# Optimization experiments

Hardware: AMD Instinct MI355X
Metric: run time of the kernel (lower is better)

The kernel has to match this reference:

```python
import jax, jax.numpy as jnp
import numpy as np

V, E, H, O = 50000, 300, 1024, 5
B, T = 64, 512


def setup_inputs() -> dict:
    key = jax.random.key(0)
    ks = jax.random.split(key, 8)
    s_ih = 1.0 / np.sqrt(H)
    return {
        "x": jax.random.randint(ks[0], (B, T), 0, V, dtype=jnp.int32),
        "embeddings": jax.random.normal(ks[1], (V, E), dtype=jnp.float32),
        "W_ih": jax.random.uniform(ks[2], (3 * H, E), jnp.float32, -s_ih, s_ih),
        "W_hh": jax.random.uniform(ks[3], (3 * H, H), jnp.float32, -s_ih, s_ih),
        "b_ih": jax.random.uniform(ks[4], (3 * H,), jnp.float32, -s_ih, s_ih),
        "b_hh": jax.random.uniform(ks[5], (3 * H,), jnp.float32, -s_ih, s_ih),
        "W_fc": jax.random.uniform(ks[6], (O, H), jnp.float32, -s_ih, s_ih),
        "b_fc": jax.random.uniform(ks[7], (O,), jnp.float32, -s_ih, s_ih),
    }


def _gru_last_hidden(emb, W_ih, W_hh, b_ih, b_hh):
    # emb: [B, T, E] -> last hidden state [B, H]
    Hd = W_hh.shape[1]
    # Precompute input contributions for all timesteps: [B, T, 3H]
    gx_all = jnp.einsum("bte,ge->btg", emb, W_ih) + b_ih
    gx_all = jnp.swapaxes(gx_all, 0, 1)  # [T, B, 3H] for scan

    def step(h, gx):
        gh = h @ W_hh.T + b_hh  # [B, 3H]
        xr, xz, xn = jnp.split(gx, 3, axis=-1)
        hr, hz, hn = jnp.split(gh, 3, axis=-1)
        r = jax.nn.sigmoid(xr + hr)
        z = jax.nn.sigmoid(xz + hz)
        n = jnp.tanh(xn + r * hn)
        h_new = (1.0 - z) * n + z * h
        return h_new, None

    h0 = jnp.zeros((emb.shape[0], Hd), dtype=emb.dtype)
    h_last, _ = jax.lax.scan(step, h0, gx_all)
    return h_last


def reference(x, embeddings, W_ih, W_hh, b_ih, b_hh, W_fc, b_fc):
    emb = embeddings[x]  # [B, T, E] embedding lookup (frozen table)
    h_last = _gru_last_hidden(emb, W_ih, W_hh, b_ih, b_hh)  # [B, H]
    return h_last @ W_fc.T + b_fc  # [B, O]
```

## Files before the change

### kernel.cpp

```cpp
#include <hip/hip_runtime.h>
#include <hip/hip_bf16.h>

typedef unsigned short u16;
typedef unsigned long long u64;
typedef __attribute__((ext_vector_type(8))) short bf16x8;
typedef __attribute__((ext_vector_type(4))) float f32x4;

#define MFMA16(a, b, c) __builtin_amdgcn_mfma_f32_16x16x32_bf16((a), (b), (c), 0, 0, 0)

static constexpr int Ee = 300, EP = 320, Hh = 1024, G3 = 3072;
static constexpr int Bb = 64, Tt = 512;

static constexpr long OFF_GX   = 0L;
static constexpr long OFF_EMB  = 201326592L;
static constexpr long OFF_WIH  = 222298112L;
static constexpr long OFF_WHH  = 224264192L;
static constexpr long OFF_HBUF = 230555648L;
static constexpr long OFF_FLAG = 230817792L;

__device__ __forceinline__ u16 f2bf(float f) {
    union { float f; unsigned u; } v; v.f = f;
    unsigned u = v.u;
    return (u16)((u + 0x7fffu + ((u >> 16) & 1u)) >> 16);
}
__device__ __forceinline__ float bf2f(u16 u) {
    union { unsigned u; float f; } v; v.u = ((unsigned)u) << 16;
    return v.f;
}
__device__ __forceinline__ float fast_sigmoid(float x) {
    return 1.f / (1.f + __expf(-x));
}
__device__ __forceinline__ float fast_tanh(float x) {
    float ax = fabsf(x);
    float e = __expf(-2.f * ax);
    float t = (1.f - e) / (1.f + e);
    return copysignf(t, x);
}

static constexpr long R0 = (long)Bb * Tt * EP;
static constexpr long R1 = (long)G3 * EP;
static constexpr long R2 = (long)G3 * Hh;
static constexpr long R3 = 131072;
static constexpr long R4 = 1024;
static constexpr long R5 = 320;

__global__ void prep_kernel(const int* __restrict__ x, const float* __restrict__ emb,
                            const float* __restrict__ wih, const float* __restrict__ whh,
                            const float* __restrict__ bfc,
                            u16* __restrict__ emb_bf, u16* __restrict__ wih_bf,
                            u16* __restrict__ whh_bf, u16* __restrict__ h0,
                            int* __restrict__ cnt, float* __restrict__ out) {
    const long total = R0 + R1 + R2 + R3 + R4 + R5;
    for (long i = (long)blockIdx.x * blockDim.x + threadIdx.x; i < total;
         i += (long)gridDim.x * blockDim.x) {
        if (i < R0) {
            const int m = (int)(i / EP), k = (int)(i % EP);
            const int b = m & 63, t = m >> 6;
            u16 v = 0;
            if (k < Ee) {
                const int xi = x[b * Tt + t];
                v = f2bf(emb[(size_t)xi * Ee + k]);
            }
            emb_bf[i] = v;
        } else if (i < R0 + R1) {
            const long j = i - R0;
            const int k = (int)(j % EP);
            const int n = (int)(j / EP);
            wih_bf[j] = (k < Ee) ? f2bf(wih[(size_t)n * Ee + k]) : (u16)0;
        } else if (i < R0 + R1 + R2) {
            const long j = i - R0 - R1;
            whh_bf[j] = f2bf(whh[j]);
        } else if (i < R0 + R1 + R2 + R3) {
            h0[i - R0 - R1 - R2] = 0;
        } else if (i < R0 + R1 + R2 + R3 + R4) {
            cnt[i - R0 - R1 - R2 - R3] = 0;
        } else {
            const long j = i - R0 - R1 - R2 - R3 - R4;
            out[j] = bfc[j % 5];
        }
    }
}

__global__ __launch_bounds__(256, 2)
void gx_gemm(const u16* __restrict__ A, const u16* __restrict__ Bm,
             const float* __restrict__ bih, u16* __restrict__ gx) {
    __shared__ __align__(16) u16 lA[128 * 32];
    __shared__ __align__(16) u16 lB[128 * 32];
    const int tid = threadIdx.x;
    const int lane = tid & 63;
    const int wv = tid >> 6;
    const int quad = lane >> 4, l15 = lane & 15;
    const int m0 = blockIdx.x * 128;
    const int n0 = blockIdx.y * 128;
    const int mo = (wv & 1) * 64, no = (wv >> 1) * 64;
    const int srow = tid >> 2;
    const int sseg = tid & 3;

    f32x4 acc[4][4] = {};

    for (int s = 0; s < 10; ++s) {
        const int k0 = s * 32;
        __syncthreads();
#pragma unroll
        for (int p = 0; p < 2; ++p) {
            const u16* ga = A + (size_t)(m0 + p * 64 + srow) * EP + k0 + sseg * 8;
            u16* la = &lA[p * 2048 + wv * 512];
            __builtin_amdgcn_global_load_lds(
                (const __attribute__((address_space(1))) void*)ga,
                (__attribute__((address_space(3))) void*)la, 16, 0, 0);
            const u16* gb = Bm + (size_t)(n0 + p * 64 + srow) * EP + k0 + sseg * 8;
            u16* lb = &lB[p * 2048 + wv * 512];
            __builtin_amdgcn_global_load_lds(
                (const __attribute__((address_space(1))) void*)gb,
                (__attribute__((address_space(3))) void*)lb, 16, 0, 0);
        }
        __syncthreads();

        bf16x8 af[4], bfr[4];
#pragma unroll
        for (int mt = 0; mt < 4; ++mt)
            af[mt] = *(const bf16x8*)&lA[(mo + mt * 16 + l15) * 32 + quad * 8];
#pragma unroll
        for (int nt = 0; nt < 4; ++nt)
            bfr[nt] = *(const bf16x8*)&lB[(no + nt * 16 + l15) * 32 + quad * 8];
#pragma unroll
        for (int mt = 0; mt < 4; ++mt)
#pragma unroll
            for (int nt = 0; nt < 4; ++nt)
                acc[mt][nt] = MFMA16(af[mt], bfr[nt], acc[mt][nt]);
    }

#pragma unroll
    for (int mt = 0; mt < 4; ++mt) {
        const int mg = m0 + mo + mt * 16 + quad * 4;
        const int t = mg >> 6, b0 = mg & 63;
#pragma unroll
        for (int nt = 0; nt < 4; ++nt) {
            const int n = n0 + no + nt * 16 + l15;
            const float bi = bih[n];
            ushort4 vv;
            vv.x = f2bf(acc[mt][nt][0] + bi);
            vv.y = f2bf(acc[mt][nt][1] + bi);
            vv.z = f2bf(acc[mt][nt][2] + bi);
            vv.w = f2bf(acc[mt][nt][3] + bi);
            *(ushort4*)&gx[((size_t)t * G3 + n) * 64 + b0] = vv;
        }
    }
}

__global__ __launch_bounds__(512, 2)
void scan_kernel(const u16* __restrict__ whh, const float* __restrict__ bhh,
                 const u16* __restrict__ gx, u16* __restrict__ hbuf,
                 const float* __restrict__ wfc, float* __restrict__ out,
                 int* __restrict__ cnt) {
    __shared__ __align__(16) u16 lh[16 * 1032];
    __shared__ __align__(16) float red[2][3][4][256];

    const int bid = blockIdx.x;
    const int bg = bid >> 5;
    const int cg = bid & 31;
    const int w = threadIdx.x >> 6;
    const int lane = threadIdx.x & 63;
    const int kq = w & 3;
    const int nh = w >> 2;
    const int quad = lane >> 4, l15 = lane & 15;
    const int c0 = cg * 32;
    const bool isLoader = (nh == 0);
    const bool isGate = (w == 3) || (w == 4);
    const int gnh = (w == 3) ? 0 : 1;

    bf16x8 wf[3][8];
#pragma unroll
    for (int g = 0; g < 3; ++g) {
        const size_t rbase = (size_t)(g * 1024 + c0 + nh * 16 + l15) * 1024;
#pragma unroll
        for (int s = 0; s < 8; ++s)
            wf[g][s] = *(const bf16x8*)&whh[rbase + (kq * 8 + s) * 32 + quad * 8];
    }

    float bh[3][4];
    u16 gxv[3][4];
    float hO[4] = {0.f, 0.f, 0.f, 0.f};
    if (isGate) {
#pragma unroll
        for (int g = 0; g < 3; ++g)
#pragma unroll
            for (int jj = 0; jj < 4; ++jj) {
                const int jglob = c0 + gnh * 16 + quad * 4 + jj;
                bh[g][jj] = bhh[g * 1024 + jglob];
                gxv[g][jj] = gx[((size_t)0 * G3 + g * 1024 + jglob) * 64 + bg * 16 + l15];
            }
    }

    u16* hb = hbuf + bg * 32768;
    int* mycnt = &cnt[bg * 16];

    for (int t = 0; t < 512; ++t) {
        const u16* hc = hb + (t & 1) * 16384;
        u16* hn = hb + ((t + 1) & 1) * 16384;

        if (isLoader) {
            u64 stg[16];
            const u64* src = (const u64*)hc + kq * 1024 + lane;
#pragma unroll
            for (int r = 0; r < 16; ++r)
                stg[r] = __hip_atomic_load(src + r * 64, __ATOMIC_RELAXED,
                                           __HIP_MEMORY_SCOPE_AGENT);
#pragma unroll
            for (int r = 0; r < 16; ++r) {
                const int row = kq * 4 + (r >> 2);
                const int col = (r & 3) * 256 + lane * 4;
                *(u64*)&lh[row * 1032 + col] = stg[r];
            }
        }
        __syncthreads();

        bf16x8 af[8];
#pragma unroll
        for (int s = 0; s < 8; ++s)
            af[s] = *(const bf16x8*)&lh[l15 * 1032 + kq * 256 + s * 32 + quad * 8];
        f32x4 acc[3] = {};
#pragma unroll
        for (int s = 0; s < 8; ++s) {
            acc[0] = MFMA16(af[s], wf[0][s], acc[0]);
            acc[1] = MFMA16(af[s], wf[1][s], acc[1]);
            acc[2] = MFMA16(af[s], wf[2][s], acc[2]);
        }
#pragma unroll
        for (int g = 0; g < 3; ++g)
            *(f32x4*)&red[nh][g][kq][quad * 64 + l15 * 4] = acc[g];
        __syncthreads();

        if (isGate) {
            const int eb = (l15 >> 2) * 64 + quad * 16 + (l15 & 3);
            u64 pack = 0;
#pragma unroll
            for (int jj = 0; jj < 4; ++jj) {
                const int e = eb + jj * 4;
                const float s0 = red[gnh][0][0][e] + red[gnh][0][1][e] +
                                 red[gnh][0][2][e] + red[gnh][0][3][e];
                const float s1 = red[gnh][1][0][e] + red[gnh][1][1][e] +
                                 red[gnh][1][2][e] + red[gnh][1][3][e];
                const float s2 = red[gnh][2][0][e] + red[gnh][2][1][e] +
                                 red[gnh][2][2][e] + red[gnh][2][3][e];
                const float rg = fast_sigmoid(bf2f(gxv[0][jj]) + s0 + bh[0][jj]);
                const float zg = fast_sigmoid(bf2f(gxv[1][jj]) + s1 + bh[1][jj]);
                const float ng = fast_tanh(bf2f(gxv[2][jj]) + rg * (s2 + bh[2][jj]));
                const float hv = (1.f - zg) * ng + zg * hO[jj];
                hO[jj] = hv;
                pack |= (u64)f2bf(hv) << (jj * 16);
            }
            __hip_atomic_store((u64*)&hn[l15 * 1024 + c0 + gnh * 16 + quad * 4],
                               pack, __ATOMIC_RELAXED, __HIP_MEMORY_SCOPE_AGENT);
            if (t < 511) {
#pragma unroll
                for (int g = 0; g < 3; ++g)
#pragma unroll
                    for (int jj = 0; jj < 4; ++jj)
                        gxv[g][jj] = gx[((size_t)(t + 1) * G3 + g * 1024 + c0 +
                                         gnh * 16 + quad * 4 + jj) * 64 + bg * 16 + l15];
            }
        }
        __syncthreads();
        if (threadIdx.x == 0) atomicAdd(mycnt, 1);
        if (isLoader && t < 511) {
            if (lane == 0) {
                while (__hip_atomic_load(mycnt, __ATOMIC_RELAXED,
                                         __HIP_MEMORY_SCOPE_AGENT) < 32 * (t + 1)) {}
            }
        }
    }

    if (isGate) {
#pragma unroll
        for (int p = 0; p < 5; ++p) {
            float v = 0.f;
#pragma unroll
            for (int jj = 0; jj < 4; ++jj)
                v += hO[jj] * wfc[p * 1024 + c0 + gnh * 16 + quad * 4 + jj];
            v += __shfl_xor(v, 16);
            v += __shfl_xor(v, 32);
            if (quad == 0)
                atomicAdd(&out[(bg * 16 + l15) * 5 + p], v);
        }
    }
}

extern "C" void kernel_launch(void* const* d_in, const int* in_sizes, int n_in,
                              void* d_out, int out_size, void* d_ws, size_t ws_size,
                              hipStream_t stream) {
    const int*   x   = (const int*)d_in[0];
    const float* emb = (const float*)d_in[1];
    const float* wih = (const float*)d_in[2];
    const float* whh = (const float*)d_in[3];
    const float* bih = (const float*)d_in[4];
    const float* bhh = (const float*)d_in[5];
    const float* wfc = (const float*)d_in[6];
    const float* bfc = (const float*)d_in[7];
    float* out = (float*)d_out;

    char* ws = (char*)d_ws;
    u16*   gxw   = (u16*)(ws + OFF_GX);
    u16*   embbf = (u16*)(ws + OFF_EMB);
    u16*   wihbf = (u16*)(ws + OFF_WIH);
    u16*   whhbf = (u16*)(ws + OFF_WHH);
    u16*   hbuf  = (u16*)(ws + OFF_HBUF);
    int*   cnt   = (int*)(ws + OFF_FLAG);

    prep_kernel<<<8192, 256, 0, stream>>>(x, emb, wih, whh, bfc, embbf, wihbf,
                                          whhbf, hbuf, cnt, out);

    gx_gemm<<<dim3(256, 24), 256, 0, stream>>>(embbf, wihbf, bih, gxw);

    scan_kernel<<<128, 512, 0, stream>>>(whhbf, bhh, gxw, hbuf, wfc, out, cnt);
}
```

Baseline: 2.326 ms.

## Replace counter barrier with tag bits embedded in hidden-state words

Drops the global atomic counter and spin-wait between timesteps. Each packed 4-element hidden-state word now carries a parity tag in the LSB of its first bf16, and all threads poll their own words until the tag matches. This folds data and flag into one load. The reduction buffer is also padded and read as vectors, and all 512 threads share the loading. The cost is a perturbed LSB of one bf16 per group, which adds a little precision error, and more threads polling global memory.

New measurement: 2.645 ms. 1.14x slower.

```diff
diff --git a/kernel.cpp b/kernel.cpp
--- a/kernel.cpp
+++ b/kernel.cpp
@@ -16,7 +16,6 @@
 static constexpr long OFF_WIH  = 222298112L;
 static constexpr long OFF_WHH  = 224264192L;
 static constexpr long OFF_HBUF = 230555648L;
-static constexpr long OFF_FLAG = 230817792L;
 
 __device__ __forceinline__ u16 f2bf(float f) {
     union { float f; unsigned u; } v; v.f = f;
@@ -41,16 +40,15 @@
 static constexpr long R1 = (long)G3 * EP;
 static constexpr long R2 = (long)G3 * Hh;
 static constexpr long R3 = 131072;
-static constexpr long R4 = 1024;
-static constexpr long R5 = 320;
+static constexpr long R4 = 320;
 
 __global__ void prep_kernel(const int* __restrict__ x, const float* __restrict__ emb,
                             const float* __restrict__ wih, const float* __restrict__ whh,
                             const float* __restrict__ bfc,
                             u16* __restrict__ emb_bf, u16* __restrict__ wih_bf,
                             u16* __restrict__ whh_bf, u16* __restrict__ h0,
-                            int* __restrict__ cnt, float* __restrict__ out) {
-    const long total = R0 + R1 + R2 + R3 + R4 + R5;
+                            float* __restrict__ out) {
+    const long total = R0 + R1 + R2 + R3 + R4;
     for (long i = (long)blockIdx.x * blockDim.x + threadIdx.x; i < total;
          i += (long)gridDim.x * blockDim.x) {
         if (i < R0) {
@@ -71,11 +69,11 @@
             const long j = i - R0 - R1;
             whh_bf[j] = f2bf(whh[j]);
         } else if (i < R0 + R1 + R2 + R3) {
-            h0[i - R0 - R1 - R2] = 0;
-        } else if (i < R0 + R1 + R2 + R3 + R4) {
-            cnt[i - R0 - R1 - R2 - R3] = 0;
+            const long idx = i - R0 - R1 - R2;
+            const int slot = (int)((idx >> 14) & 1);
+            h0[idx] = (slot == 1 && (idx & 3) == 0) ? (u16)1 : (u16)0;
         } else {
-            const long j = i - R0 - R1 - R2 - R3 - R4;
+            const long j = i - R0 - R1 - R2 - R3;
             out[j] = bfc[j % 5];
         }
     }
@@ -151,10 +149,9 @@
 __global__ __launch_bounds__(512, 2)
 void scan_kernel(const u16* __restrict__ whh, const float* __restrict__ bhh,
                  const u16* __restrict__ gx, u16* __restrict__ hbuf,
-                 const float* __restrict__ wfc, float* __restrict__ out,
-                 int* __restrict__ cnt) {
+                 const float* __restrict__ wfc, float* __restrict__ out) {
     __shared__ __align__(16) u16 lh[16 * 1032];
-    __shared__ __align__(16) float red[2][3][4][256];
+    __shared__ __align__(16) float red[2][3][4][16 * 20];
 
     const int bid = blockIdx.x;
     const int bg = bid >> 5;
@@ -165,7 +162,6 @@
     const int nh = w >> 2;
     const int quad = lane >> 4, l15 = lane & 15;
     const int c0 = cg * 32;
-    const bool isLoader = (nh == 0);
     const bool isGate = (w == 3) || (w == 4);
     const int gnh = (w == 3) ? 0 : 1;
 
@@ -188,31 +184,38 @@
             for (int jj = 0; jj < 4; ++jj) {
                 const int jglob = c0 + gnh * 16 + quad * 4 + jj;
                 bh[g][jj] = bhh[g * 1024 + jglob];
-                gxv[g][jj] = gx[((size_t)0 * G3 + g * 1024 + jglob) * 64 + bg * 16 + l15];
-            }
-    }
-
-    u16* hb = hbuf + bg * 32768;
-    int* mycnt = &cnt[bg * 16];
+                gxv[g][jj] = gx[((size_t)g * 1024 + jglob) * 64 + bg * 16 + l15];
+            }
+    }
+
+    u64* hbq = (u64*)hbuf + (size_t)bg * 8192;
+    const int srow = threadIdx.x >> 5;
+    const int scol = threadIdx.x & 31;
+    u64* lhq = (u64*)lh;
 
     for (int t = 0; t < 512; ++t) {
-        const u16* hc = hb + (t & 1) * 16384;
-        u16* hn = hb + ((t + 1) & 1) * 16384;
-
-        if (isLoader) {
-            u64 stg[16];
-            const u64* src = (const u64*)hc + kq * 1024 + lane;
-#pragma unroll
-            for (int r = 0; r < 16; ++r)
-                stg[r] = __hip_atomic_load(src + r * 64, __ATOMIC_RELAXED,
-                                           __HIP_MEMORY_SCOPE_AGENT);
-#pragma unroll
-            for (int r = 0; r < 16; ++r) {
-                const int row = kq * 4 + (r >> 2);
-                const int col = (r & 3) * 256 + lane * 4;
-                *(u64*)&lh[row * 1032 + col] = stg[r];
-            }
-        }
+        const u64* hcq = hbq + (t & 1) * 4096;
+        u16* hn = hbuf + (size_t)bg * 32768 + ((t + 1) & 1) * 16384;
+        const unsigned et = (unsigned)((t >> 1) & 1);
+
+        u64 stg[8];
+        unsigned need = 0xFFu;
+        while (need) {
+            unsigned got = 0;
+#pragma unroll
+            for (int r = 0; r < 8; ++r) {
+                if (need & (1u << r)) {
+                    u64 v = __hip_atomic_load(&hcq[srow * 256 + scol + 32 * r],
+                                              __ATOMIC_RELAXED, __HIP_MEMORY_SCOPE_AGENT);
+                    stg[r] = v;
+                    if ((unsigned)(v & 1ull) == et) got |= 1u << r;
+                }
+            }
+            need &= ~got;
+        }
+#pragma unroll
+        for (int r = 0; r < 8; ++r)
+            lhq[srow * 258 + scol + 32 * r] = stg[r];
         __syncthreads();
 
         bf16x8 af[8];
@@ -228,27 +231,37 @@
         }
 #pragma unroll
         for (int g = 0; g < 3; ++g)
-            *(f32x4*)&red[nh][g][kq][quad * 64 + l15 * 4] = acc[g];
-        __syncthreads();
-
+#pragma unroll
+            for (int r = 0; r < 4; ++r)
+                red[nh][g][kq][(quad * 4 + r) * 20 + l15] = acc[g][r];
+        __syncthreads();
+
+        f32x4 rr[3][4];
         if (isGate) {
-            const int eb = (l15 >> 2) * 64 + quad * 16 + (l15 & 3);
+#pragma unroll
+            for (int g = 0; g < 3; ++g)
+#pragma unroll
+                for (int k = 0; k < 4; ++k)
+                    rr[g][k] = *(const f32x4*)&red[gnh][g][k][l15 * 20 + quad * 4];
+        }
+        __syncthreads();
+
+        if (isGate) {
+            const unsigned wtag = (unsigned)(((t + 1) >> 1) & 1);
             u64 pack = 0;
 #pragma unroll
             for (int jj = 0; jj < 4; ++jj) {
-                const int e = eb + jj * 4;
-                const float s0 = red[gnh][0][0][e] + red[gnh][0][1][e] +
-                                 red[gnh][0][2][e] + red[gnh][0][3][e];
-                const float s1 = red[gnh][1][0][e] + red[gnh][1][1][e] +
-                                 red[gnh][1][2][e] + red[gnh][1][3][e];
-                const float s2 = red[gnh][2][0][e] + red[gnh][2][1][e] +
-                                 red[gnh][2][2][e] + red[gnh][2][3][e];
+                const float s0 = rr[0][0][jj] + rr[0][1][jj] + rr[0][2][jj] + rr[0][3][jj];
+                const float s1 = rr[1][0][jj] + rr[1][1][jj] + rr[1][2][jj] + rr[1][3][jj];
+                const float s2 = rr[2][0][jj] + rr[2][1][jj] + rr[2][2][jj] + rr[2][3][jj];
                 const float rg = fast_sigmoid(bf2f(gxv[0][jj]) + s0 + bh[0][jj]);
                 const float zg = fast_sigmoid(bf2f(gxv[1][jj]) + s1 + bh[1][jj]);
                 const float ng = fast_tanh(bf2f(gxv[2][jj]) + rg * (s2 + bh[2][jj]));
                 const float hv = (1.f - zg) * ng + zg * hO[jj];
                 hO[jj] = hv;
-                pack |= (u64)f2bf(hv) << (jj * 16);
+                u16 hb16 = f2bf(hv);
+                if (jj == 0) hb16 = (u16)((hb16 & ~1u) | wtag);
+                pack |= (u64)hb16 << (jj * 16);
             }
             __hip_atomic_store((u64*)&hn[l15 * 1024 + c0 + gnh * 16 + quad * 4],
                                pack, __ATOMIC_RELAXED, __HIP_MEMORY_SCOPE_AGENT);
@@ -259,14 +272,6 @@
                     for (int jj = 0; jj < 4; ++jj)
                         gxv[g][jj] = gx[((size_t)(t + 1) * G3 + g * 1024 + c0 +
                                          gnh * 16 + quad * 4 + jj) * 64 + bg * 16 + l15];
-            }
-        }
-        __syncthreads();
-        if (threadIdx.x == 0) atomicAdd(mycnt, 1);
-        if (isLoader && t < 511) {
-            if (lane == 0) {
-                while (__hip_atomic_load(mycnt, __ATOMIC_RELAXED,
-                                         __HIP_MEMORY_SCOPE_AGENT) < 32 * (t + 1)) {}
             }
         }
     }
@@ -305,12 +310,11 @@
     u16*   wihbf = (u16*)(ws + OFF_WIH);
     u16*   whhbf = (u16*)(ws + OFF_WHH);
     u16*   hbuf  = (u16*)(ws + OFF_HBUF);
-    int*   cnt   = (int*)(ws + OFF_FLAG);
 
     prep_kernel<<<8192, 256, 0, stream>>>(x, emb, wih, whh, bfc, embbf, wihbf,
-                                          whhbf, hbuf, cnt, out);
+                                          whhbf, hbuf, out);
 
     gx_gemm<<<dim3(256, 24), 256, 0, stream>>>(embbf, wihbf, bih, gxw);
 
-    scan_kernel<<<128, 512, 0, stream>>>(whhbf, bhh, gxw, hbuf, wfc, out, cnt);
-}
+    scan_kernel<<<128, 512, 0, stream>>>(whhbf, bhh, gxw, hbuf, wfc, out);
+}
```
